# Optimization experiments

Measured on AMD Instinct MI355X. Metric: run time of the kernel, lower is better.

## Reference

```python
import jax, jax.numpy as jnp
import numpy as np

EPS = 1e-5  # torch.nn.LayerNorm default
NUM_HEADS = 8


def _layernorm(x, g, b):
    mu = jnp.mean(x, axis=-1, keepdims=True)
    var = jnp.mean((x - mu) ** 2, axis=-1, keepdims=True)
    return (x - mu) * jax.lax.rsqrt(var + EPS) * g + b


def setup_inputs() -> dict:
    key = jax.random.key(0)
    ks = jax.random.split(key, 8)
    B, S, D = 4, 2048, 512
    scale = 0.02
    return {
        'x': jax.random.normal(ks[0], (B, S, D), dtype=jnp.float32),
        'gene_types': jax.random.randint(ks[1], (B, S), 0, 2),
        'tf_g': jnp.ones((D,), jnp.float32), 'tf_b': jnp.zeros((D,), jnp.float32),
        'tg_g': jnp.ones((D,), jnp.float32), 'tg_b': jnp.zeros((D,), jnp.float32),
        'in_proj_w': jax.random.normal(ks[2], (3 * D, D), dtype=jnp.float32) * scale,
        'in_proj_b': jnp.zeros((3 * D,), jnp.float32),
        'out_proj_w': jax.random.normal(ks[3], (D, D), dtype=jnp.float32) * scale,
        'out_proj_b': jnp.zeros((D,), jnp.float32),
        'w1': jax.random.normal(ks[4], (D // 2, D), dtype=jnp.float32) * scale,
        'b1': jnp.zeros((D // 2,), jnp.float32),
        'w2': jax.random.normal(ks[5], (1, D // 2), dtype=jnp.float32) * scale,
        'b2': jnp.zeros((1,), jnp.float32),
    }


def reference(x, gene_types, tf_g, tf_b, tg_g, tg_b,
              in_proj_w, in_proj_b, out_proj_w, out_proj_b,
              w1, b1, w2, b2):
    B, S, D = x.shape
    H = NUM_HEADS
    HD = D // H
    # --- vectorized per-token conditional LayerNorm (gene_type 0 -> tf, 1 -> target, else passthrough) ---
    gt = gene_types[..., None]
    xn = jnp.where(gt == 0, _layernorm(x, tf_g, tf_b),
                   jnp.where(gt == 1, _layernorm(x, tg_g, tg_b), x))
    # --- multi-head self-attention (torch MultiheadAttention, batch_first) ---
    qkv = xn @ in_proj_w.T + in_proj_b            # [B,S,3D]
    q, k, v = jnp.split(qkv, 3, axis=-1)
    to_heads = lambda t: t.reshape(B, S, H, HD).transpose(0, 2, 1, 3)  # [B,H,S,HD]
    q, k, v = to_heads(q), to_heads(k), to_heads(v)
    scores = jnp.einsum('bhqd,bhkd->bhqk', q, k) / jnp.sqrt(jnp.float32(HD))
    attn = jax.nn.softmax(scores, axis=-1)
    o = jnp.einsum('bhqk,bhkd->bhqd', attn, v)
    o = o.transpose(0, 2, 1, 3).reshape(B, S, D)
    o = o @ out_proj_w.T + out_proj_b
    xr = xn + o                                    # residual
    # --- regulatory strength gate: Linear -> SiLU -> Linear -> Sigmoid ---
    h = jax.nn.silu(xr @ w1.T + b1)                # [B,S,D/2]
    strength = jax.nn.sigmoid(h @ w2.T + b2)       # [B,S,1]
    return xr * strength
```

## Files before the change

kernel.cpp:

```cpp
#include <hip/hip_runtime.h>

typedef __bf16 bf16;
typedef __bf16 bf16x4_t __attribute__((ext_vector_type(4)));
typedef __bf16 bf16x8_t __attribute__((ext_vector_type(8)));
typedef float f32x4_t __attribute__((ext_vector_type(4)));

#define MFMA16(a, b, c) __builtin_amdgcn_mfma_f32_16x16x32_bf16(a, b, c, 0, 0, 0)

static __device__ __forceinline__ f32x4_t mfma_k16(bf16x4_t a, bf16x4_t b, f32x4_t c) {
#if __has_builtin(__builtin_amdgcn_mfma_f32_16x16x16bf16_1k)
    typedef short s16x4_t __attribute__((ext_vector_type(4)));
    return __builtin_amdgcn_mfma_f32_16x16x16bf16_1k(
        __builtin_bit_cast(s16x4_t, a), __builtin_bit_cast(s16x4_t, b), c, 0, 0, 0);
#else
    bf16x8_t az = {}, bz = {};
    az[0] = a[0]; az[1] = a[1]; az[2] = a[2]; az[3] = a[3];
    bz[0] = b[0]; bz[1] = b[1]; bz[2] = b[2]; bz[3] = b[3];
    return MFMA16(az, bz, c);
#endif
}

__global__ void cast3_k(const float* __restrict__ a, const float* __restrict__ b,
                        const float* __restrict__ c, bf16* __restrict__ da,
                        bf16* __restrict__ db, bf16* __restrict__ dc) {
    int i = blockIdx.x * blockDim.x + threadIdx.x;
    if (i < 786432) da[i] = (bf16)a[i];
    else if (i < 1048576) db[i - 786432] = (bf16)b[i - 786432];
    else if (i < 1179648) dc[i - 1048576] = (bf16)c[i - 1048576];
}

__global__ __launch_bounds__(256) void ln_k(const float* __restrict__ x,
                                            const int* __restrict__ gt,
                                            const float* __restrict__ tfg,
                                            const float* __restrict__ tfb,
                                            const float* __restrict__ tgg,
                                            const float* __restrict__ tgb,
                                            bf16* __restrict__ xn) {
    int wid = threadIdx.x >> 6, lane = threadIdx.x & 63;
    int t = blockIdx.x * 4 + wid;
    const float4* xr = (const float4*)(x + (size_t)t * 512);
    float4 a = xr[lane * 2], b = xr[lane * 2 + 1];
    float s = (a.x + a.y) + (a.z + a.w) + (b.x + b.y) + (b.z + b.w);
    float sq = a.x * a.x + a.y * a.y + a.z * a.z + a.w * a.w +
               b.x * b.x + b.y * b.y + b.z * b.z + b.w * b.w;
    for (int m = 1; m < 64; m <<= 1) {
        s += __shfl_xor(s, m, 64);
        sq += __shfl_xor(sq, m, 64);
    }
    float mean = s * (1.f / 512.f);
    float var = fmaxf(sq * (1.f / 512.f) - mean * mean, 0.f);
    float rstd = rsqrtf(var + 1e-5f);
    int g = gt[t];
    float4 o0, o1;
    if (g < 2) {
        const float4* gp = (const float4*)(g ? tgg : tfg);
        const float4* bp = (const float4*)(g ? tgb : tfb);
        float4 g0 = gp[lane * 2], g1 = gp[lane * 2 + 1];
        float4 b0 = bp[lane * 2], b1 = bp[lane * 2 + 1];
        o0.x = (a.x - mean) * rstd * g0.x + b0.x;
        o0.y = (a.y - mean) * rstd * g0.y + b0.y;
        o0.z = (a.z - mean) * rstd * g0.z + b0.z;
        o0.w = (a.w - mean) * rstd * g0.w + b0.w;
        o1.x = (b.x - mean) * rstd * g1.x + b1.x;
        o1.y = (b.y - mean) * rstd * g1.y + b1.y;
        o1.z = (b.z - mean) * rstd * g1.z + b1.z;
        o1.w = (b.w - mean) * rstd * g1.w + b1.w;
    } else {
        o0 = a; o1 = b;
    }
    bf16* xo = xn + (size_t)t * 512 + lane * 8;
    bf16x4_t p0, p1;
    p0[0] = (bf16)o0.x; p0[1] = (bf16)o0.y; p0[2] = (bf16)o0.z; p0[3] = (bf16)o0.w;
    p1[0] = (bf16)o1.x; p1[1] = (bf16)o1.y; p1[2] = (bf16)o1.z; p1[3] = (bf16)o1.w;
    *(bf16x4_t*)xo = p0;
    *(bf16x4_t*)(xo + 4) = p1;
}

template <int EPI>
__global__ __launch_bounds__(256) void gemm_k(const bf16* __restrict__ A,
                                              const bf16* __restrict__ B,
                                              const float* __restrict__ bias,
                                              bf16* __restrict__ p0,
                                              bf16* __restrict__ p1,
                                              bf16* __restrict__ p2,
                                              const bf16* __restrict__ xn,
                                              float* __restrict__ xrf) {
    int m0 = blockIdx.x * 128, n0 = blockIdx.y * 128;
    int tid = threadIdx.x;
    int lane = tid & 63, w = tid >> 6;
    int quad = lane >> 4, l15 = lane & 15;
    int wm = (w >> 1) * 64, wn = (w & 1) * 64;
    __shared__ bf16 As[128 * 72];
    __shared__ bf16 Bs[128 * 72];
    f32x4_t acc[4][4] = {};
    int srow = tid >> 3, ssub = tid & 7;
    const bf16* Ab = A + (size_t)(m0 + srow) * 512 + ssub * 8;
    const bf16* Bb = B + (size_t)(n0 + srow) * 512 + ssub * 8;
    uint4 pa[4], pb[4];
    auto gload = [&](int s) {
        int k0 = s * 64;
#pragma unroll
        for (int i = 0; i < 4; ++i) {
            pa[i] = *(const uint4*)(Ab + (size_t)(i * 32) * 512 + k0);
            pb[i] = *(const uint4*)(Bb + (size_t)(i * 32) * 512 + k0);
        }
    };
    auto sstore = [&]() {
#pragma unroll
        for (int i = 0; i < 4; ++i) {
            *(uint4*)&As[(i * 32 + srow) * 72 + ssub * 8] = pa[i];
            *(uint4*)&Bs[(i * 32 + srow) * 72 + ssub * 8] = pb[i];
        }
    };
    gload(0);
    sstore();
    for (int s = 0; s < 8; ++s) {
        __syncthreads();
        if (s < 7) gload(s + 1);
#pragma unroll
        for (int ks = 0; ks < 2; ++ks) {
            bf16x8_t af[4], bfr[4];
            int koff = ks * 32 + quad * 8;
#pragma unroll
            for (int mt = 0; mt < 4; ++mt)
                af[mt] = *(const bf16x8_t*)&As[(wm + mt * 16 + l15) * 72 + koff];
#pragma unroll
            for (int nt = 0; nt < 4; ++nt)
                bfr[nt] = *(const bf16x8_t*)&Bs[(wn + nt * 16 + l15) * 72 + koff];
#pragma unroll
            for (int mt = 0; mt < 4; ++mt)
#pragma unroll
                for (int nt = 0; nt < 4; ++nt)
                    acc[mt][nt] = MFMA16(af[mt], bfr[nt], acc[mt][nt]);
        }
        __syncthreads();
        if (s < 7) sstore();
    }
#pragma unroll
    for (int mt = 0; mt < 4; ++mt) {
#pragma unroll
        for (int nt = 0; nt < 4; ++nt) {
            int gcol = n0 + wn + nt * 16 + l15;
            float bcol = bias[gcol];
#pragma unroll
            for (int r = 0; r < 4; ++r) {
                int grow = m0 + wm + mt * 16 + quad * 4 + r;
                float v = acc[mt][nt][r] + bcol;
                if constexpr (EPI == 0) {
                    int which = gcol >> 9;
                    int d = gcol & 511;
                    int hh = d >> 6, hd = d & 63;
                    int b = grow >> 11, ssi = grow & 2047;
                    size_t bh = (size_t)(b * 8 + hh);
                    if (which == 0) {
                        p0[(bh * 2048 + ssi) * 64 + hd] = (bf16)(v * 0.180336880111f);
                    } else if (which == 1) {
                        p1[(bh * 2048 + ssi) * 64 + hd] = (bf16)v;
                    } else {
                        p2[(bh * 64 + hd) * 2048 + ssi] = (bf16)v;
                    }
                } else if constexpr (EPI == 1) {
                    size_t idx = (size_t)grow * 512 + gcol;
                    float xv = v + (float)xn[idx];
                    xrf[idx] = xv;
                    p0[idx] = (bf16)xv;
                } else {
                    float sv = v / (1.f + __expf(-v));
                    p0[(size_t)grow * 256 + gcol] = (bf16)sv;
                }
            }
        }
    }
    (void)p1; (void)p2; (void)xn; (void)xrf;
}

__global__ __launch_bounds__(256) void attn_k(const bf16* __restrict__ q,
                                              const bf16* __restrict__ k,
                                              const bf16* __restrict__ vt,
                                              bf16* __restrict__ pO,
                                              float* __restrict__ pL,
                                              int nsplit) {
    int bh = blockIdx.y;
    int q0 = blockIdx.x * 128;
    int sz = blockIdx.z;
    int tiles = 32 / nsplit;
    int kt0 = sz * tiles;
    int tid = threadIdx.x;
    int lane = tid & 63, w = tid >> 6;
    int quad = lane >> 4, l15 = lane & 15;
    __shared__ bf16 Ks[64 * 72];
    __shared__ bf16 Vs[64 * 72];
    const bf16* qb = q + (size_t)bh * 2048 * 64;
    const bf16* kb = k + (size_t)bh * 2048 * 64;
    const bf16* vb = vt + (size_t)bh * 64 * 2048;
    bf16x8_t qf[2][2];
#pragma unroll
    for (int qt = 0; qt < 2; ++qt)
#pragma unroll
        for (int ks = 0; ks < 2; ++ks)
            qf[qt][ks] = *(const bf16x8_t*)(qb + (size_t)(q0 + w * 32 + qt * 16 + l15) * 64 + ks * 32 + quad * 8);
    bf16x4_t ones4;
#pragma unroll
    for (int i = 0; i < 4; ++i) ones4[i] = (bf16)1.0f;
    f32x4_t oacc[2][4] = {};
    f32x4_t lacc[2] = {};
    int srow = tid >> 3, ssub = tid & 7;
    uint4 pk[2], pv[2];
    auto gload = [&](int kt) {
        int kbase = kt * 64;
#pragma unroll
        for (int i = 0; i < 2; ++i) {
            int row = i * 32 + srow;
            pk[i] = *(const uint4*)(kb + (size_t)(kbase + row) * 64 + ssub * 8);
            pv[i] = *(const uint4*)(vb + (size_t)row * 2048 + kbase + ssub * 8);
        }
    };
    auto sstore = [&]() {
#pragma unroll
        for (int i = 0; i < 2; ++i) {
            int row = i * 32 + srow;
            *(uint4*)&Ks[row * 72 + ssub * 8] = pk[i];
            *(uint4*)&Vs[row * 72 + ssub * 8] = pv[i];
        }
    };
    gload(kt0);
    for (int kt = kt0; kt < kt0 + tiles; ++kt) {
        __syncthreads();
        sstore();
        __syncthreads();
        if (kt + 1 < kt0 + tiles) gload(kt + 1);
        f32x4_t sacc[4][2] = {};
#pragma unroll
        for (int ks = 0; ks < 2; ++ks) {
            int koff = ks * 32 + quad * 8;
            bf16x8_t kf[4];
#pragma unroll
            for (int nt = 0; nt < 4; ++nt)
                kf[nt] = *(const bf16x8_t*)&Ks[(nt * 16 + l15) * 72 + koff];
#pragma unroll
            for (int nt = 0; nt < 4; ++nt)
#pragma unroll
                for (int qt = 0; qt < 2; ++qt)
                    sacc[nt][qt] = MFMA16(kf[nt], qf[qt][ks], sacc[nt][qt]);
        }
        bf16x4_t pf[4][2];
#pragma unroll
        for (int nt = 0; nt < 4; ++nt)
#pragma unroll
            for (int qt = 0; qt < 2; ++qt)
#pragma unroll
                for (int r = 0; r < 4; ++r)
                    pf[nt][qt][r] = (bf16)exp2f(sacc[nt][qt][r]);
#pragma unroll
        for (int nt = 0; nt < 4; ++nt) {
            bf16x4_t vf[4];
#pragma unroll
            for (int dt = 0; dt < 4; ++dt)
                vf[dt] = *(const bf16x4_t*)&Vs[(dt * 16 + l15) * 72 + nt * 16 + quad * 4];
#pragma unroll
            for (int qt = 0; qt < 2; ++qt) {
#pragma unroll
                for (int dt = 0; dt < 4; ++dt)
                    oacc[qt][dt] = mfma_k16(pf[nt][qt], vf[dt], oacc[qt][dt]);
                lacc[qt] = mfma_k16(pf[nt][qt], ones4, lacc[qt]);
            }
        }
    }
    size_t obase = ((size_t)(sz * 32 + bh) * 2048 + q0);
#pragma unroll
    for (int qt = 0; qt < 2; ++qt)
#pragma unroll
        for (int r = 0; r < 4; ++r) {
            int row = w * 32 + qt * 16 + quad * 4 + r;
#pragma unroll
            for (int dt = 0; dt < 4; ++dt)
                pO[(obase + row) * 64 + dt * 16 + l15] = (bf16)oacc[qt][dt][r];
            if (l15 == 0) pL[obase + row] = lacc[qt][r];
        }
}

__global__ __launch_bounds__(256) void comb_k(const bf16* __restrict__ pO,
                                              const float* __restrict__ pL,
                                              bf16* __restrict__ o, int nsplit) {
    int i = blockIdx.x * 256 + threadIdx.x;
    int hd = (i & 15) * 4;
    int s = (i >> 4) & 2047;
    int bh = i >> 15;
    float l = 0.f;
    float acc[4] = {};
    for (int sp = 0; sp < nsplit; ++sp) {
        size_t r = (size_t)(sp * 32 + bh) * 2048 + s;
        l += pL[r];
        bf16x4_t a = *(const bf16x4_t*)(pO + r * 64 + hd);
#pragma unroll
        for (int j = 0; j < 4; ++j) acc[j] += (float)a[j];
    }
    float inv = 1.f / l;
    int bb = bh >> 3, hh = bh & 7;
    bf16x4_t ov;
#pragma unroll
    for (int j = 0; j < 4; ++j) ov[j] = (bf16)(acc[j] * inv);
    *(bf16x4_t*)(o + ((size_t)(bb * 2048 + s) * 512) + hh * 64 + hd) = ov;
}

__global__ __launch_bounds__(256) void gate_k(const bf16* __restrict__ h,
                                              const float* __restrict__ w2,
                                              const float* __restrict__ b2,
                                              const float* __restrict__ xrf,
                                              float* __restrict__ out) {
    int t = blockIdx.x * 4 + (threadIdx.x >> 6);
    int lane = threadIdx.x & 63;
    const bf16* hr = h + (size_t)t * 256;
    bf16x4_t hv = *(const bf16x4_t*)(hr + lane * 4);
    float4 wv = *(const float4*)(w2 + lane * 4);
    float dot = (float)hv[0] * wv.x + (float)hv[1] * wv.y + (float)hv[2] * wv.z + (float)hv[3] * wv.w;
    for (int m = 1; m < 64; m <<= 1) dot += __shfl_xor(dot, m, 64);
    float st = 1.f / (1.f + __expf(-(dot + b2[0])));
    const float4* x4 = (const float4*)(xrf + (size_t)t * 512);
    float4* o4 = (float4*)(out + (size_t)t * 512);
#pragma unroll
    for (int j = 0; j < 2; ++j) {
        float4 xv = x4[lane * 2 + j];
        float4 ov;
        ov.x = xv.x * st; ov.y = xv.y * st; ov.z = xv.z * st; ov.w = xv.w * st;
        o4[lane * 2 + j] = ov;
    }
}

extern "C" void kernel_launch(void* const* d_in, const int* in_sizes, int n_in,
                              void* d_out, int out_size, void* d_ws, size_t ws_size,
                              hipStream_t stream) {
    const float* x    = (const float*)d_in[0];
    const int*   gt   = (const int*)d_in[1];
    const float* tfg  = (const float*)d_in[2];
    const float* tfb  = (const float*)d_in[3];
    const float* tgg  = (const float*)d_in[4];
    const float* tgb  = (const float*)d_in[5];
    const float* Wqkv = (const float*)d_in[6];
    const float* bqkv = (const float*)d_in[7];
    const float* Wout = (const float*)d_in[8];
    const float* bout = (const float*)d_in[9];
    const float* W1   = (const float*)d_in[10];
    const float* b1   = (const float*)d_in[11];
    const float* w2   = (const float*)d_in[12];
    const float* b2   = (const float*)d_in[13];
    float* out = (float*)d_out;
    char* ws = (char*)d_ws;

    const size_t MB = 1024 * 1024;
    bf16*  wq  = (bf16*)(ws + 0);
    bf16*  wo  = (bf16*)(ws + 1536 * 512 * 2);
    bf16*  w1b = (bf16*)(ws + (1536 + 512) * 512 * 2);
    float* pL  = (float*)(ws + 2304 * 512 * 2);
    bf16*  xn  = (bf16*)(ws + 4 * MB);
    bf16*  q   = (bf16*)(ws + 12 * MB);
    bf16*  o   = (bf16*)(ws + 12 * MB);
    bf16*  kk  = (bf16*)(ws + 20 * MB);
    bf16*  vt  = (bf16*)(ws + 28 * MB);
    float* xrf = (float*)(ws + 20 * MB);
    bf16*  pO  = (bf16*)(ws + 36 * MB);
    bf16*  xrb = (bf16*)(ws + 36 * MB);
    bf16*  h   = (bf16*)(ws + 44 * MB);

    int nsplit = (ws_size >= 69 * MB) ? 4 : 2;

    cast3_k<<<4608, 256, 0, stream>>>(Wqkv, Wout, W1, wq, wo, w1b);
    ln_k<<<2048, 256, 0, stream>>>(x, gt, tfg, tfb, tgg, tgb, xn);
    gemm_k<0><<<dim3(64, 12), 256, 0, stream>>>(xn, wq, bqkv, q, kk, vt, nullptr, nullptr);
    attn_k<<<dim3(16, 32, nsplit), 256, 0, stream>>>(q, kk, vt, pO, pL, nsplit);
    comb_k<<<4096, 256, 0, stream>>>(pO, pL, o, nsplit);
    gemm_k<1><<<dim3(64, 4), 256, 0, stream>>>(o, wo, bout, xrb, nullptr, nullptr, xn, xrf);
    gemm_k<2><<<dim3(64, 2), 256, 0, stream>>>(xrb, w1b, b1, h, nullptr, nullptr, nullptr, nullptr);
    gate_k<<<2048, 256, 0, stream>>>(h, w2, b2, xrf, out);
    (void)in_sizes; (void)n_in; (void)out_size;
}
```

Measured before the change: 345.0 us.

## Fuse kernels: cast+LN, split-combine into out-proj, MLP with gate

Merges the weight cast and LayerNorm into one launch. It folds the attention split-combine (normalising by the summed row sums) into the out-projection GEMM's A-tile load, and fuses the W1 GEMM, SiLU, the w2 dot, the sigmoid and the final scaling into a single MLP kernel. This removes intermediate buffers (o, h) and three launches. In exchange, nsplit is fixed at 2, which lowers attention parallelism on the 4-split path, and the MLP kernel uses only 256 blocks with a full 256-column weight tile.

```diff
diff --git a/kernel.cpp b/kernel.cpp
--- a/kernel.cpp
+++ b/kernel.cpp
@@ -20,24 +20,28 @@
 #endif
 }
 
-__global__ void cast3_k(const float* __restrict__ a, const float* __restrict__ b,
-                        const float* __restrict__ c, bf16* __restrict__ da,
-                        bf16* __restrict__ db, bf16* __restrict__ dc) {
-    int i = blockIdx.x * blockDim.x + threadIdx.x;
-    if (i < 786432) da[i] = (bf16)a[i];
-    else if (i < 1048576) db[i - 786432] = (bf16)b[i - 786432];
-    else if (i < 1179648) dc[i - 1048576] = (bf16)c[i - 1048576];
-}
-
-__global__ __launch_bounds__(256) void ln_k(const float* __restrict__ x,
-                                            const int* __restrict__ gt,
-                                            const float* __restrict__ tfg,
-                                            const float* __restrict__ tfb,
-                                            const float* __restrict__ tgg,
-                                            const float* __restrict__ tgb,
-                                            bf16* __restrict__ xn) {
+__global__ __launch_bounds__(256) void castln_k(const float* __restrict__ Wqkv,
+                                                const float* __restrict__ Wout,
+                                                const float* __restrict__ W1,
+                                                bf16* __restrict__ wq,
+                                                bf16* __restrict__ wo,
+                                                bf16* __restrict__ w1b,
+                                                const float* __restrict__ x,
+                                                const int* __restrict__ gt,
+                                                const float* __restrict__ tfg,
+                                                const float* __restrict__ tfb,
+                                                const float* __restrict__ tgg,
+                                                const float* __restrict__ tgb,
+                                                bf16* __restrict__ xn) {
+    if (blockIdx.x < 4608) {
+        int i = blockIdx.x * 256 + threadIdx.x;
+        if (i < 786432) wq[i] = (bf16)Wqkv[i];
+        else if (i < 1048576) wo[i - 786432] = (bf16)Wout[i - 786432];
+        else if (i < 1179648) w1b[i - 1048576] = (bf16)W1[i - 1048576];
+        return;
+    }
     int wid = threadIdx.x >> 6, lane = threadIdx.x & 63;
-    int t = blockIdx.x * 4 + wid;
+    int t = (blockIdx.x - 4608) * 4 + wid;
     const float4* xr = (const float4*)(x + (size_t)t * 512);
     float4 a = xr[lane * 2], b = xr[lane * 2 + 1];
     float s = (a.x + a.y) + (a.z + a.w) + (b.x + b.y) + (b.z + b.w);
@@ -76,15 +80,12 @@
     *(bf16x4_t*)(xo + 4) = p1;
 }
 
-template <int EPI>
-__global__ __launch_bounds__(256) void gemm_k(const bf16* __restrict__ A,
-                                              const bf16* __restrict__ B,
-                                              const float* __restrict__ bias,
-                                              bf16* __restrict__ p0,
-                                              bf16* __restrict__ p1,
-                                              bf16* __restrict__ p2,
-                                              const bf16* __restrict__ xn,
-                                              float* __restrict__ xrf) {
+__global__ __launch_bounds__(256) void gemmqkv_k(const bf16* __restrict__ A,
+                                                 const bf16* __restrict__ B,
+                                                 const float* __restrict__ bias,
+                                                 bf16* __restrict__ q,
+                                                 bf16* __restrict__ kk,
+                                                 bf16* __restrict__ vt) {
     int m0 = blockIdx.x * 128, n0 = blockIdx.y * 128;
     int tid = threadIdx.x;
     int lane = tid & 63, w = tid >> 6;
@@ -146,45 +147,32 @@
             for (int r = 0; r < 4; ++r) {
                 int grow = m0 + wm + mt * 16 + quad * 4 + r;
                 float v = acc[mt][nt][r] + bcol;
-                if constexpr (EPI == 0) {
-                    int which = gcol >> 9;
-                    int d = gcol & 511;
-                    int hh = d >> 6, hd = d & 63;
-                    int b = grow >> 11, ssi = grow & 2047;
-                    size_t bh = (size_t)(b * 8 + hh);
-                    if (which == 0) {
-                        p0[(bh * 2048 + ssi) * 64 + hd] = (bf16)(v * 0.180336880111f);
-                    } else if (which == 1) {
-                        p1[(bh * 2048 + ssi) * 64 + hd] = (bf16)v;
-                    } else {
-                        p2[(bh * 64 + hd) * 2048 + ssi] = (bf16)v;
-                    }
-                } else if constexpr (EPI == 1) {
-                    size_t idx = (size_t)grow * 512 + gcol;
-                    float xv = v + (float)xn[idx];
-                    xrf[idx] = xv;
-                    p0[idx] = (bf16)xv;
+                int which = gcol >> 9;
+                int d = gcol & 511;
+                int hh = d >> 6, hd = d & 63;
+                int b = grow >> 11, ssi = grow & 2047;
+                size_t bh = (size_t)(b * 8 + hh);
+                if (which == 0) {
+                    q[(bh * 2048 + ssi) * 64 + hd] = (bf16)(v * 0.180336880111f);
+                } else if (which == 1) {
+                    kk[(bh * 2048 + ssi) * 64 + hd] = (bf16)v;
                 } else {
-                    float sv = v / (1.f + __expf(-v));
-                    p0[(size_t)grow * 256 + gcol] = (bf16)sv;
+                    vt[(bh * 64 + hd) * 2048 + ssi] = (bf16)v;
                 }
             }
         }
     }
-    (void)p1; (void)p2; (void)xn; (void)xrf;
 }
 
 __global__ __launch_bounds__(256) void attn_k(const bf16* __restrict__ q,
                                               const bf16* __restrict__ k,
                                               const bf16* __restrict__ vt,
                                               bf16* __restrict__ pO,
-                                              float* __restrict__ pL,
-                                              int nsplit) {
+                                              float* __restrict__ pL) {
     int bh = blockIdx.y;
     int q0 = blockIdx.x * 128;
     int sz = blockIdx.z;
-    int tiles = 32 / nsplit;
-    int kt0 = sz * tiles;
+    const int kt0 = sz * 16;
     int tid = threadIdx.x;
     int lane = tid & 63, w = tid >> 6;
     int quad = lane >> 4, l15 = lane & 15;
@@ -224,11 +212,11 @@
         }
     };
     gload(kt0);
-    for (int kt = kt0; kt < kt0 + tiles; ++kt) {
+    for (int kt = kt0; kt < kt0 + 16; ++kt) {
         __syncthreads();
         sstore();
         __syncthreads();
-        if (kt + 1 < kt0 + tiles) gload(kt + 1);
+        if (kt + 1 < kt0 + 16) gload(kt + 1);
         f32x4_t sacc[4][2] = {};
 #pragma unroll
         for (int ks = 0; ks < 2; ++ks) {
@@ -279,51 +267,190 @@
         }
 }
 
-__global__ __launch_bounds__(256) void comb_k(const bf16* __restrict__ pO,
-                                              const float* __restrict__ pL,
-                                              bf16* __restrict__ o, int nsplit) {
-    int i = blockIdx.x * 256 + threadIdx.x;
-    int hd = (i & 15) * 4;
-    int s = (i >> 4) & 2047;
-    int bh = i >> 15;
-    float l = 0.f;
-    float acc[4] = {};
-    for (int sp = 0; sp < nsplit; ++sp) {
-        size_t r = (size_t)(sp * 32 + bh) * 2048 + s;
-        l += pL[r];
-        bf16x4_t a = *(const bf16x4_t*)(pO + r * 64 + hd);
-#pragma unroll
-        for (int j = 0; j < 4; ++j) acc[j] += (float)a[j];
-    }
-    float inv = 1.f / l;
-    int bb = bh >> 3, hh = bh & 7;
-    bf16x4_t ov;
-#pragma unroll
-    for (int j = 0; j < 4; ++j) ov[j] = (bf16)(acc[j] * inv);
-    *(bf16x4_t*)(o + ((size_t)(bb * 2048 + s) * 512) + hh * 64 + hd) = ov;
-}
-
-__global__ __launch_bounds__(256) void gate_k(const bf16* __restrict__ h,
-                                              const float* __restrict__ w2,
-                                              const float* __restrict__ b2,
-                                              const float* __restrict__ xrf,
-                                              float* __restrict__ out) {
-    int t = blockIdx.x * 4 + (threadIdx.x >> 6);
-    int lane = threadIdx.x & 63;
-    const bf16* hr = h + (size_t)t * 256;
-    bf16x4_t hv = *(const bf16x4_t*)(hr + lane * 4);
-    float4 wv = *(const float4*)(w2 + lane * 4);
-    float dot = (float)hv[0] * wv.x + (float)hv[1] * wv.y + (float)hv[2] * wv.z + (float)hv[3] * wv.w;
-    for (int m = 1; m < 64; m <<= 1) dot += __shfl_xor(dot, m, 64);
-    float st = 1.f / (1.f + __expf(-(dot + b2[0])));
-    const float4* x4 = (const float4*)(xrf + (size_t)t * 512);
-    float4* o4 = (float4*)(out + (size_t)t * 512);
-#pragma unroll
-    for (int j = 0; j < 2; ++j) {
-        float4 xv = x4[lane * 2 + j];
+__global__ __launch_bounds__(256) void gemmo_k(const bf16* __restrict__ pO,
+                                               const float* __restrict__ pL,
+                                               const bf16* __restrict__ B,
+                                               const float* __restrict__ bias,
+                                               const bf16* __restrict__ xn,
+                                               bf16* __restrict__ xrb,
+                                               float* __restrict__ xrf) {
+    int m0 = blockIdx.x * 128, n0 = blockIdx.y * 128;
+    int tid = threadIdx.x;
+    int lane = tid & 63, w = tid >> 6;
+    int quad = lane >> 4, l15 = lane & 15;
+    int wm = (w >> 1) * 64, wn = (w & 1) * 64;
+    __shared__ bf16 As[128 * 72];
+    __shared__ bf16 Bs[128 * 72];
+    f32x4_t acc[4][4] = {};
+    int srow = tid >> 3, ssub = tid & 7;
+    const bf16* Bb = B + (size_t)(n0 + srow) * 512 + ssub * 8;
+    bf16x8_t pa[4];
+    uint4 pb[4];
+    auto gload = [&](int s) {
+        int k0 = s * 64;
+#pragma unroll
+        for (int i = 0; i < 4; ++i) {
+            int t = m0 + i * 32 + srow;
+            int b = t >> 11, ssi = t & 2047;
+            size_t r0 = ((size_t)(b * 8 + s)) * 2048 + ssi;
+            size_t r1 = ((size_t)(32 + b * 8 + s)) * 2048 + ssi;
+            float inv = 1.f / (pL[r0] + pL[r1]);
+            bf16x8_t a0 = *(const bf16x8_t*)(pO + r0 * 64 + ssub * 8);
+            bf16x8_t a1 = *(const bf16x8_t*)(pO + r1 * 64 + ssub * 8);
+            bf16x8_t c;
+#pragma unroll
+            for (int j = 0; j < 8; ++j) c[j] = (bf16)(((float)a0[j] + (float)a1[j]) * inv);
+            pa[i] = c;
+            pb[i] = *(const uint4*)(Bb + (size_t)(i * 32) * 512 + k0);
+        }
+    };
+    auto sstore = [&]() {
+#pragma unroll
+        for (int i = 0; i < 4; ++i) {
+            *(bf16x8_t*)&As[(i * 32 + srow) * 72 + ssub * 8] = pa[i];
+            *(uint4*)&Bs[(i * 32 + srow) * 72 + ssub * 8] = pb[i];
+        }
+    };
+    gload(0);
+    sstore();
+    for (int s = 0; s < 8; ++s) {
+        __syncthreads();
+        if (s < 7) gload(s + 1);
+#pragma unroll
+        for (int ks = 0; ks < 2; ++ks) {
+            bf16x8_t af[4], bfr[4];
+            int koff = ks * 32 + quad * 8;
+#pragma unroll
+            for (int mt = 0; mt < 4; ++mt)
+                af[mt] = *(const bf16x8_t*)&As[(wm + mt * 16 + l15) * 72 + koff];
+#pragma unroll
+            for (int nt = 0; nt < 4; ++nt)
+                bfr[nt] = *(const bf16x8_t*)&Bs[(wn + nt * 16 + l15) * 72 + koff];
+#pragma unroll
+            for (int mt = 0; mt < 4; ++mt)
+#pragma unroll
+                for (int nt = 0; nt < 4; ++nt)
+                    acc[mt][nt] = MFMA16(af[mt], bfr[nt], acc[mt][nt]);
+        }
+        __syncthreads();
+        if (s < 7) sstore();
+    }
+#pragma unroll
+    for (int mt = 0; mt < 4; ++mt) {
+#pragma unroll
+        for (int nt = 0; nt < 4; ++nt) {
+            int gcol = n0 + wn + nt * 16 + l15;
+            float bcol = bias[gcol];
+#pragma unroll
+            for (int r = 0; r < 4; ++r) {
+                int grow = m0 + wm + mt * 16 + quad * 4 + r;
+                size_t idx = (size_t)grow * 512 + gcol;
+                float xv = acc[mt][nt][r] + bcol + (float)xn[idx];
+                xrf[idx] = xv;
+                xrb[idx] = (bf16)xv;
+            }
+        }
+    }
+}
+
+__global__ __launch_bounds__(256) void mlp_k(const bf16* __restrict__ A,
+                                             const bf16* __restrict__ B,
+                                             const float* __restrict__ b1,
+                                             const float* __restrict__ w2,
+                                             const float* __restrict__ b2,
+                                             const float* __restrict__ xrf,
+                                             float* __restrict__ out) {
+    int m0 = blockIdx.x * 32;
+    int tid = threadIdx.x;
+    int lane = tid & 63, w = tid >> 6;
+    int quad = lane >> 4, l15 = lane & 15;
+    int wn = w * 64;
+    __shared__ bf16 As[32 * 72];
+    __shared__ bf16 Bs[256 * 72];
+    __shared__ float red[4][32];
+    __shared__ float st[32];
+    f32x4_t acc[2][4] = {};
+    int srow = tid >> 3, ssub = tid & 7;
+    uint4 pa, pb[8];
+    auto gload = [&](int s) {
+        int k0 = s * 64;
+        pa = *(const uint4*)(A + (size_t)(m0 + srow) * 512 + ssub * 8 + k0);
+#pragma unroll
+        for (int i = 0; i < 8; ++i)
+            pb[i] = *(const uint4*)(B + (size_t)(i * 32 + srow) * 512 + ssub * 8 + k0);
+    };
+    auto sstore = [&]() {
+        *(uint4*)&As[srow * 72 + ssub * 8] = pa;
+#pragma unroll
+        for (int i = 0; i < 8; ++i)
+            *(uint4*)&Bs[(i * 32 + srow) * 72 + ssub * 8] = pb[i];
+    };
+    gload(0);
+    sstore();
+    for (int s = 0; s < 8; ++s) {
+        __syncthreads();
+        if (s < 7) gload(s + 1);
+#pragma unroll
+        for (int ks = 0; ks < 2; ++ks) {
+            int koff = ks * 32 + quad * 8;
+            bf16x8_t af[2], bfr[4];
+#pragma unroll
+            for (int mt = 0; mt < 2; ++mt)
+                af[mt] = *(const bf16x8_t*)&As[(mt * 16 + l15) * 72 + koff];
+#pragma unroll
+            for (int nt = 0; nt < 4; ++nt)
+                bfr[nt] = *(const bf16x8_t*)&Bs[(wn + nt * 16 + l15) * 72 + koff];
+#pragma unroll
+            for (int mt = 0; mt < 2; ++mt)
+#pragma unroll
+                for (int nt = 0; nt < 4; ++nt)
+                    acc[mt][nt] = MFMA16(af[mt], bfr[nt], acc[mt][nt]);
+        }
+        __syncthreads();
+        if (s < 7) sstore();
+    }
+    f32x4_t ds[2] = {};
+#pragma unroll
+    for (int mt = 0; mt < 2; ++mt)
+#pragma unroll
+        for (int nt = 0; nt < 4; ++nt) {
+            int gcol = wn + nt * 16 + l15;
+            float bb = b1[gcol], ww = w2[gcol];
+#pragma unroll
+            for (int r = 0; r < 4; ++r) {
+                float v = acc[mt][nt][r] + bb;
+                float sv = v / (1.f + __expf(-v));
+                ds[mt][r] += sv * ww;
+            }
+        }
+#pragma unroll
+    for (int m = 1; m < 16; m <<= 1)
+#pragma unroll
+        for (int mt = 0; mt < 2; ++mt)
+#pragma unroll
+            for (int r = 0; r < 4; ++r) ds[mt][r] += __shfl_xor(ds[mt][r], m, 64);
+    if (l15 == 0) {
+#pragma unroll
+        for (int mt = 0; mt < 2; ++mt)
+#pragma unroll
+            for (int r = 0; r < 4; ++r) red[w][mt * 16 + quad * 4 + r] = ds[mt][r];
+    }
+    __syncthreads();
+    if (tid < 32) {
+        float d = red[0][tid] + red[1][tid] + red[2][tid] + red[3][tid] + b2[0];
+        st[tid] = 1.f / (1.f + __expf(-d));
+    }
+    __syncthreads();
+    int row = tid >> 3, seg = tid & 7;
+    float sr = st[row];
+    const float4* x4 = (const float4*)(xrf + (size_t)(m0 + row) * 512);
+    float4* o4 = (float4*)(out + (size_t)(m0 + row) * 512);
+#pragma unroll
+    for (int jj = 0; jj < 16; ++jj) {
+        float4 xv = x4[jj * 8 + seg];
         float4 ov;
-        ov.x = xv.x * st; ov.y = xv.y * st; ov.z = xv.z * st; ov.w = xv.w * st;
-        o4[lane * 2 + j] = ov;
+        ov.x = xv.x * sr; ov.y = xv.y * sr; ov.z = xv.z * sr; ov.w = xv.w * sr;
+        o4[jj * 8 + seg] = ov;
     }
 }
 
@@ -354,23 +481,17 @@
     float* pL  = (float*)(ws + 2304 * 512 * 2);
     bf16*  xn  = (bf16*)(ws + 4 * MB);
     bf16*  q   = (bf16*)(ws + 12 * MB);
-    bf16*  o   = (bf16*)(ws + 12 * MB);
+    bf16*  xrb = (bf16*)(ws + 12 * MB);
     bf16*  kk  = (bf16*)(ws + 20 * MB);
     bf16*  vt  = (bf16*)(ws + 28 * MB);
-    float* xrf = (float*)(ws + 20 * MB);
     bf16*  pO  = (bf16*)(ws + 36 * MB);
-    bf16*  xrb = (bf16*)(ws + 36 * MB);
-    bf16*  h   = (bf16*)(ws + 44 * MB);
-
-    int nsplit = (ws_size >= 69 * MB) ? 4 : 2;
-
-    cast3_k<<<4608, 256, 0, stream>>>(Wqkv, Wout, W1, wq, wo, w1b);
-    ln_k<<<2048, 256, 0, stream>>>(x, gt, tfg, tfb, tgg, tgb, xn);
-    gemm_k<0><<<dim3(64, 12), 256, 0, stream>>>(xn, wq, bqkv, q, kk, vt, nullptr, nullptr);
-    attn_k<<<dim3(16, 32, nsplit), 256, 0, stream>>>(q, kk, vt, pO, pL, nsplit);
-    comb_k<<<4096, 256, 0, stream>>>(pO, pL, o, nsplit);
-    gemm_k<1><<<dim3(64, 4), 256, 0, stream>>>(o, wo, bout, xrb, nullptr, nullptr, xn, xrf);
-    gemm_k<2><<<dim3(64, 2), 256, 0, stream>>>(xrb, w1b, b1, h, nullptr, nullptr, nullptr, nullptr);
-    gate_k<<<2048, 256, 0, stream>>>(h, w2, b2, xrf, out);
-    (void)in_sizes; (void)n_in; (void)out_size;
-}
+    float* xrf = (float*)(ws + 52 * MB);
+
+    castln_k<<<6656, 256, 0, stream>>>(Wqkv, Wout, W1, wq, wo, w1b,
+                                       x, gt, tfg, tfb, tgg, tgb, xn);
+    gemmqkv_k<<<dim3(64, 12), 256, 0, stream>>>(xn, wq, bqkv, q, kk, vt);
+    attn_k<<<dim3(16, 32, 2), 256, 0, stream>>>(q, kk, vt, pO, pL);
+    gemmo_k<<<dim3(64, 4), 256, 0, stream>>>(pO, pL, wo, bout, xn, xrb, xrf);
+    mlp_k<<<256, 256, 0, stream>>>(xrb, w1b, b1, w2, b2, xrf, out);
+    (void)in_sizes; (void)n_in; (void)out_size; (void)ws_size;
+}
```

After: 336.1 us. -2.6%, faster.
